# Optimization experiments

Measured on AMD Instinct MI355X. Metric: run time of the kernel, lower is better.

The kernel has to match this reference:

```python
import jax, jax.numpy as jnp
import numpy as np

N_NODES = 100000
N_EDGES = 1200000
IN_CH = 64
HID = 64


def sage_conv(x, src, dst, Wl, b, Wr, num_nodes):
    # mean aggregation of source-node features at target nodes (flow=source_to_target)
    msg = x[src]                                      # [E, C] gather
    agg = jax.ops.segment_sum(msg, dst, num_segments=num_nodes)  # [N, C]
    cnt = jax.ops.segment_sum(jnp.ones((src.shape[0],), x.dtype), dst,
                              num_segments=num_nodes)
    mean = agg / jnp.maximum(cnt, 1.0)[:, None]
    # PyG SAGEConv: lin_l(aggregated) + bias + lin_r(root)
    return mean @ Wl + b + x @ Wr


def setup_inputs() -> dict:
    key = jax.random.key(0)
    ks = jax.random.split(key, 10)
    x = jax.random.normal(ks[0], (N_NODES, IN_CH), dtype=jnp.float32)
    edge_index = jax.random.randint(ks[1], (2, N_EDGES), 0, N_NODES, dtype=jnp.int64)
    s1 = 1.0 / np.sqrt(IN_CH)
    s2 = 1.0 / np.sqrt(HID)
    W1l = jax.random.uniform(ks[2], (IN_CH, HID), jnp.float32, -s1, s1)
    b1 = jax.random.uniform(ks[3], (HID,), jnp.float32, -s1, s1)
    W1r = jax.random.uniform(ks[4], (IN_CH, HID), jnp.float32, -s1, s1)
    W2l = jax.random.uniform(ks[5], (HID, HID), jnp.float32, -s2, s2)
    b2 = jax.random.uniform(ks[6], (HID,), jnp.float32, -s2, s2)
    W2r = jax.random.uniform(ks[7], (HID, HID), jnp.float32, -s2, s2)
    Wfc = jax.random.uniform(ks[8], (HID, 1), jnp.float32, -s2, s2)
    bfc = jax.random.uniform(ks[9], (1,), jnp.float32, -s2, s2)
    return {"x": x, "edge_index": edge_index, "W1l": W1l, "b1": b1, "W1r": W1r,
            "W2l": W2l, "b2": b2, "W2r": W2r, "Wfc": Wfc, "bfc": bfc}


def reference(x, edge_index, W1l, b1, W1r, W2l, b2, W2r, Wfc, bfc):
    num_nodes = x.shape[0]
    src, dst = edge_index[0], edge_index[1]
    x = jnp.nan_to_num(x, nan=0.0)
    # layer 1: SAGEConv -> ReLU (dropout is identity in eval)
    h = jax.nn.relu(sage_conv(x, src, dst, W1l, b1, W1r, num_nodes))
    # layer 2
    h = jax.nn.relu(sage_conv(h, src, dst, W2l, b2, W2r, num_nodes))
    pred = (h @ Wfc + bfc)[:, 0]  # (num_nodes,)
    return pred
```

## Files before the change

### kernel.cpp

```cpp
#include <hip/hip_runtime.h>

#define NN_NODES 100000
#define NN_EDGES 1200000
#define CH 64
#define BUCKET_NODES 200
#define NBUCKETS (NN_NODES / BUCKET_NODES)
#define EPB 4096
#define PASSA_THREADS 1024
#define XCDS 8
#define PCAP 768
#define BMAX (XCDS * PCAP)

typedef __attribute__((ext_vector_type(8))) short bf16x8;
typedef __attribute__((ext_vector_type(4))) float f32x4;

__device__ __forceinline__ float nan0(float v) { return v == v ? v : 0.0f; }

__device__ __forceinline__ unsigned short f2bf(float f) {
    unsigned u = __float_as_uint(f);
    return (unsigned short)((u + 0x7fffu + ((u >> 16) & 1u)) >> 16);
}

__device__ __forceinline__ unsigned xcc_id() {
    unsigned x;
    asm volatile("s_getreg_b32 %0, hwreg(HW_REG_XCC_ID)" : "=s"(x));
    return x & (XCDS - 1);
}

__global__ __launch_bounds__(256) void convert_kernel(
    const float* __restrict__ x, unsigned short* __restrict__ xb, int n4)
{
    int i = blockIdx.x * 256 + threadIdx.x;
    if (i >= n4) return;
    float4 v = ((const float4*)x)[i];
    v.x = nan0(v.x); v.y = nan0(v.y); v.z = nan0(v.z); v.w = nan0(v.w);
    ushort4 o;
    o.x = f2bf(v.x); o.y = f2bf(v.y); o.z = f2bf(v.z); o.w = f2bf(v.w);
    ((ushort4*)xb)[i] = o;
}

__global__ __launch_bounds__(256) void wprep_kernel(
    const float* __restrict__ W1l, const float* __restrict__ W1r,
    const float* __restrict__ W2l, const float* __restrict__ W2r,
    unsigned short* __restrict__ Wt1, unsigned short* __restrict__ Wt2)
{
    int i = blockIdx.x * 256 + threadIdx.x;
    if (i >= 64 * 128) return;
    int n = i >> 7;
    int k = i & 127;
    float v1 = (k < 64) ? W1l[k * 64 + n] : W1r[(k - 64) * 64 + n];
    float v2 = (k < 64) ? W2l[k * 64 + n] : W2r[(k - 64) * 64 + n];
    Wt1[i] = f2bf(v1);
    Wt2[i] = f2bf(v2);
}

__global__ __launch_bounds__(PASSA_THREADS) void passA_kernel(
    const int* __restrict__ src, const int* __restrict__ dst,
    int* __restrict__ bcnt, unsigned int* __restrict__ bbuf, int nEdges)
{
    __shared__ int lhist[NBUCKETS];
    __shared__ int lbase[NBUCKETS];
    int tid = threadIdx.x;
    int e0 = blockIdx.x * EPB;
    unsigned xcc = xcc_id();

    for (int i = tid; i < NBUCKETS; i += PASSA_THREADS) lhist[i] = 0;
    __syncthreads();

    int dreg[4];
    #pragma unroll
    for (int r = 0; r < 4; r++) {
        int e = e0 + r * PASSA_THREADS + tid;
        if (e < nEdges) {
            int d = dst[e];
            dreg[r] = d;
            atomicAdd(&lhist[d / BUCKET_NODES], 1);
        } else {
            dreg[r] = -1;
        }
    }
    __syncthreads();

    for (int i = tid; i < NBUCKETS; i += PASSA_THREADS) {
        int c = lhist[i];
        lbase[i] = c > 0 ? atomicAdd(&bcnt[i * XCDS + xcc], c) : 0;
        lhist[i] = 0;
    }
    __syncthreads();

    #pragma unroll
    for (int r = 0; r < 4; r++) {
        int d = dreg[r];
        if (d >= 0) {
            int e = e0 + r * PASSA_THREADS + tid;
            int s = src[e];
            int b = d / BUCKET_NODES;
            int dloc = d - b * BUCKET_NODES;
            int pos = lbase[b] + atomicAdd(&lhist[b], 1);
            if (pos < PCAP)
                bbuf[((size_t)b * XCDS + xcc) * PCAP + pos] =
                    ((unsigned)dloc << 24) | (unsigned)s;
        }
    }
}

__global__ __launch_bounds__(512) void scan_bcnt_kernel(
    const int* __restrict__ bcnt, int* __restrict__ bbase,
    int* __restrict__ rowptr)
{
    __shared__ int s[512];
    int t = threadIdx.x;
    int own = 0;
    if (t < NBUCKETS) {
        #pragma unroll
        for (int x = 0; x < XCDS; x++) {
            int c = bcnt[t * XCDS + x];
            own += c < PCAP ? c : PCAP;
        }
    }
    s[t] = own;
    __syncthreads();
    for (int off = 1; off < 512; off <<= 1) {
        int v = (t >= off) ? s[t - off] : 0;
        __syncthreads();
        s[t] += v;
        __syncthreads();
    }
    if (t < NBUCKETS) bbase[t] = s[t] - own;
    if (t == NBUCKETS - 1) rowptr[NN_NODES] = s[t];
}

__global__ __launch_bounds__(256) void passB_kernel(
    const int* __restrict__ bcnt, const int* __restrict__ bbase,
    const unsigned int* __restrict__ bbuf,
    int* __restrict__ col, int* __restrict__ rowptr)
{
    __shared__ int hist[BUCKET_NODES];
    __shared__ int cur[BUCKET_NODES];
    __shared__ int sc[256];
    __shared__ unsigned int stage[BMAX];
    int b = blockIdx.x;
    int t = threadIdx.x;
    int base = bbase[b];

    for (int i = t; i < BUCKET_NODES; i += 256) hist[i] = 0;
    __syncthreads();

    int cnt = 0;
    #pragma unroll
    for (int x = 0; x < XCDS; x++) {
        int pc = bcnt[b * XCDS + x];
        if (pc > PCAP) pc = PCAP;
        const unsigned int* seg = bbuf + ((size_t)b * XCDS + x) * PCAP;
        for (int k = t; k < pc; k += 256) {
            unsigned v = seg[k];
            stage[cnt + k] = v;
            atomicAdd(&hist[v >> 24], 1);
        }
        cnt += pc;
    }
    __syncthreads();

    int own = (t < BUCKET_NODES) ? hist[t] : 0;
    sc[t] = own;
    __syncthreads();
    for (int off = 1; off < 256; off <<= 1) {
        int v = (t >= off) ? sc[t - off] : 0;
        __syncthreads();
        sc[t] += v;
        __syncthreads();
    }
    if (t < BUCKET_NODES) {
        int excl = sc[t] - own;
        rowptr[b * BUCKET_NODES + t] = base + excl;
        cur[t] = excl;
    }
    __syncthreads();

    for (int k = t; k < cnt; k += 256) {
        unsigned v = stage[k];
        int dloc = (int)(v >> 24);
        int pos = atomicAdd(&cur[dloc], 1);
        col[base + pos] = (int)(v & 0xFFFFFFu);
    }
}

__global__ __launch_bounds__(256) void gather_kernel(
    const unsigned short* __restrict__ xb,
    const int* __restrict__ rowptr, const int* __restrict__ col,
    unsigned short* __restrict__ mgb, int nNodes)
{
    int w    = threadIdx.x >> 6;
    int lane = threadIdx.x & 63;
    int sub  = lane >> 4;
    int l16  = lane & 15;
    int node = blockIdx.x * 4 + w;
    if (node >= nNodes) return;
    int r0 = rowptr[node], r1 = rowptr[node + 1];
    float a0[4] = {0, 0, 0, 0}, a1[4] = {0, 0, 0, 0};
    int i = r0 + sub;
    for (; i + 4 < r1; i += 8) {
        int s0 = col[i];
        int s1 = col[i + 4];
        uint2 u0 = *(const uint2*)(xb + (size_t)s0 * CH + l16 * 4);
        uint2 u1 = *(const uint2*)(xb + (size_t)s1 * CH + l16 * 4);
        a0[0] += __uint_as_float(u0.x << 16);
        a0[1] += __uint_as_float(u0.x & 0xffff0000u);
        a0[2] += __uint_as_float(u0.y << 16);
        a0[3] += __uint_as_float(u0.y & 0xffff0000u);
        a1[0] += __uint_as_float(u1.x << 16);
        a1[1] += __uint_as_float(u1.x & 0xffff0000u);
        a1[2] += __uint_as_float(u1.y << 16);
        a1[3] += __uint_as_float(u1.y & 0xffff0000u);
    }
    if (i < r1) {
        int s0 = col[i];
        uint2 u0 = *(const uint2*)(xb + (size_t)s0 * CH + l16 * 4);
        a0[0] += __uint_as_float(u0.x << 16);
        a0[1] += __uint_as_float(u0.x & 0xffff0000u);
        a0[2] += __uint_as_float(u0.y << 16);
        a0[3] += __uint_as_float(u0.y & 0xffff0000u);
    }
    #pragma unroll
    for (int j = 0; j < 4; j++) a0[j] += a1[j];
    #pragma unroll
    for (int j = 0; j < 4; j++) {
        a0[j] += __shfl_xor(a0[j], 16, 64);
        a0[j] += __shfl_xor(a0[j], 32, 64);
    }
    if (lane < 16) {
        int deg = r1 - r0;
        float inv = 1.0f / (float)(deg > 0 ? deg : 1);
        ushort4 o;
        o.x = f2bf(a0[0] * inv); o.y = f2bf(a0[1] * inv);
        o.z = f2bf(a0[2] * inv); o.w = f2bf(a0[3] * inv);
        *(ushort4*)(mgb + (size_t)node * CH + l16 * 4) = o;
    }
}

template<int LAYER>
__global__ __launch_bounds__(256) void dense_kernel(
    const unsigned short* __restrict__ rootb,
    const unsigned short* __restrict__ mgb,
    const unsigned short* __restrict__ Wt,
    const float* __restrict__ bias,
    const float* __restrict__ Wfc, const float* __restrict__ bfc,
    unsigned short* __restrict__ hb_out,
    float* __restrict__ out,
    int nNodes)
{
    __shared__ unsigned short sA[64][136];
    __shared__ unsigned short sW[64][136];
    __shared__ unsigned short sO[64][72];

    int tid = threadIdx.x;
    int n_base = blockIdx.x * 64;

    {
        const uint4* g = (const uint4*)Wt;
        for (int i = tid; i < 1024; i += 256) {
            int n = i >> 4;
            int c = i & 15;
            *(uint4*)&sW[n][c * 8] = g[i];
        }
    }
    {
        for (int i = tid; i < 1024; i += 256) {
            int node = i >> 4;
            int c = i & 15;
            int gn = n_base + node;
            if (gn >= nNodes) gn = nNodes - 1;
            const unsigned short* srcp = (c < 8)
                ? (mgb + (size_t)gn * CH + c * 8)
                : (rootb + (size_t)gn * CH + (c - 8) * 8);
            *(uint4*)&sA[node][c * 8] = *(const uint4*)srcp;
        }
    }
    __syncthreads();

    int wave = tid >> 6;
    int lane = tid & 63;
    int quad = lane >> 4;
    int colx = lane & 15;
    int m0 = wave * 16;

    f32x4 acc[4];
    #pragma unroll
    for (int nt = 0; nt < 4; nt++) acc[nt] = (f32x4){0.f, 0.f, 0.f, 0.f};

    #pragma unroll
    for (int ks = 0; ks < 4; ks++) {
        bf16x8 af = *(const bf16x8*)&sA[m0 + colx][ks * 32 + quad * 8];
        #pragma unroll
        for (int nt = 0; nt < 4; nt++) {
            bf16x8 bfr = *(const bf16x8*)&sW[nt * 16 + colx][ks * 32 + quad * 8];
            acc[nt] = __builtin_amdgcn_mfma_f32_16x16x32_bf16(af, bfr, acc[nt], 0, 0, 0);
        }
    }

    float bv[4];
    #pragma unroll
    for (int nt = 0; nt < 4; nt++) bv[nt] = bias[nt * 16 + colx];

    if (LAYER == 1) {
        #pragma unroll
        for (int nt = 0; nt < 4; nt++)
            #pragma unroll
            for (int r = 0; r < 4; r++) {
                float v = acc[nt][r] + bv[nt];
                v = v > 0.f ? v : 0.f;
                sO[m0 + quad * 4 + r][nt * 16 + colx] = f2bf(v);
            }
        __syncthreads();
        for (int i = tid; i < 512; i += 256) {
            int node = i >> 3;
            int c = i & 7;
            int gn = n_base + node;
            if (gn < nNodes)
                *(uint4*)(hb_out + (size_t)gn * CH + c * 8) =
                    *(const uint4*)&sO[node][c * 8];
        }
    } else {
        float wf[4];
        #pragma unroll
        for (int nt = 0; nt < 4; nt++) wf[nt] = Wfc[nt * 16 + colx];
        float bfc0 = bfc[0];
        #pragma unroll
        for (int r = 0; r < 4; r++) {
            float p = 0.f;
            #pragma unroll
            for (int nt = 0; nt < 4; nt++) {
                float v = acc[nt][r] + bv[nt];
                v = v > 0.f ? v : 0.f;
                p += v * wf[nt];
            }
            p += __shfl_xor(p, 1, 64);
            p += __shfl_xor(p, 2, 64);
            p += __shfl_xor(p, 4, 64);
            p += __shfl_xor(p, 8, 64);
            if (colx == 0) {
                int gn = n_base + m0 + quad * 4 + r;
                if (gn < nNodes) out[gn] = p + bfc0;
            }
        }
    }
}

extern "C" void kernel_launch(void* const* d_in, const int* in_sizes, int n_in,
                              void* d_out, int out_size, void* d_ws, size_t ws_size,
                              hipStream_t stream) {
    const float* x    = (const float*)d_in[0];
    const int*   ei   = (const int*)d_in[1];
    const float* W1l  = (const float*)d_in[2];
    const float* b1   = (const float*)d_in[3];
    const float* W1r  = (const float*)d_in[4];
    const float* W2l  = (const float*)d_in[5];
    const float* b2   = (const float*)d_in[6];
    const float* W2r  = (const float*)d_in[7];
    const float* Wfc  = (const float*)d_in[8];
    const float* bfc  = (const float*)d_in[9];
    float* out = (float*)d_out;

    const int N = NN_NODES;
    const int E = NN_EDGES;
    const int* src = ei;
    const int* dst = ei + E;

    char* ws = (char*)d_ws;
    unsigned short* xb  = (unsigned short*)ws;  ws += (size_t)N * CH * sizeof(unsigned short);
    unsigned short* h1b = (unsigned short*)ws;  ws += (size_t)N * CH * sizeof(unsigned short);
    unsigned short* mgb = (unsigned short*)ws;  ws += (size_t)N * CH * sizeof(unsigned short);
    unsigned short* Wt1 = (unsigned short*)ws;  ws += 64 * 128 * sizeof(unsigned short);
    unsigned short* Wt2 = (unsigned short*)ws;  ws += 64 * 128 * sizeof(unsigned short);
    int* bcnt   = (int*)ws;                     ws += (size_t)NBUCKETS * XCDS * sizeof(int);
    int* bbase  = (int*)ws;                     ws += 512 * sizeof(int);
    int* rowptr = (int*)ws;                     ws += (size_t)(N + 1) * sizeof(int);
    int* col    = (int*)ws;                     ws += (size_t)E * sizeof(int);
    unsigned int* bbuf = (unsigned int*)mgb;

    hipMemsetAsync(bcnt, 0, (size_t)NBUCKETS * XCDS * sizeof(int), stream);

    convert_kernel<<<(N * CH / 4 + 255) / 256, 256, 0, stream>>>(x, xb, N * CH / 4);
    wprep_kernel<<<32, 256, 0, stream>>>(W1l, W1r, W2l, W2r, Wt1, Wt2);
    passA_kernel<<<(E + EPB - 1) / EPB, PASSA_THREADS, 0, stream>>>(
        src, dst, bcnt, bbuf, E);
    scan_bcnt_kernel<<<1, 512, 0, stream>>>(bcnt, bbase, rowptr);
    passB_kernel<<<NBUCKETS, 256, 0, stream>>>(bcnt, bbase, bbuf, col, rowptr);

    int gblocks = (N + 3) / 4;
    int dblocks = (N + 63) / 64;

    gather_kernel<<<gblocks, 256, 0, stream>>>(xb, rowptr, col, mgb, N);
    dense_kernel<1><<<dblocks, 256, 0, stream>>>(
        xb, mgb, Wt1, b1, nullptr, nullptr, h1b, nullptr, N);
    gather_kernel<<<gblocks, 256, 0, stream>>>(h1b, rowptr, col, mgb, N);
    dense_kernel<2><<<dblocks, 256, 0, stream>>>(
        h1b, mgb, Wt2, b2, Wfc, bfc, nullptr, out, N);
}
```

Before: 227.6 us.

## Fuse neighbor mean-gather into dense MFMA kernel and vectorize edge bucketing loads

The separate gather kernel and dense kernel are merged, so each 64-node block gathers neighbor means straight into shared memory and then runs the MFMA projection. This removes the write and reread of the intermediate mean buffer and two kernel launches. The cost is that each wave now walks 16 nodes one after another, with fewer blocks in flight to hide gather latency. Separately, passA now loads dst and src as int4, four contiguous edges per thread, and bbuf gets its own workspace region instead of aliasing the mean buffer.

```diff
diff --git a/kernel.cpp b/kernel.cpp
--- a/kernel.cpp
+++ b/kernel.cpp
@@ -67,18 +67,19 @@
     for (int i = tid; i < NBUCKETS; i += PASSA_THREADS) lhist[i] = 0;
     __syncthreads();
 
-    int dreg[4];
-    #pragma unroll
-    for (int r = 0; r < 4; r++) {
-        int e = e0 + r * PASSA_THREADS + tid;
-        if (e < nEdges) {
-            int d = dst[e];
-            dreg[r] = d;
-            atomicAdd(&lhist[d / BUCKET_NODES], 1);
-        } else {
-            dreg[r] = -1;
-        }
-    }
+    int eb = e0 + tid * 4;
+    int nv = nEdges - eb;
+    if (nv > 4) nv = 4;
+    int da[4] = {-1, -1, -1, -1};
+    if (nv == 4) {
+        int4 dv = *(const int4*)(dst + eb);
+        da[0] = dv.x; da[1] = dv.y; da[2] = dv.z; da[3] = dv.w;
+    } else {
+        for (int r = 0; r < nv; r++) da[r] = dst[eb + r];
+    }
+    #pragma unroll
+    for (int r = 0; r < 4; r++)
+        if (da[r] >= 0) atomicAdd(&lhist[da[r] / BUCKET_NODES], 1);
     __syncthreads();
 
     for (int i = tid; i < NBUCKETS; i += PASSA_THREADS) {
@@ -88,18 +89,23 @@
     }
     __syncthreads();
 
+    int sa[4] = {0, 0, 0, 0};
+    if (nv == 4) {
+        int4 sv = *(const int4*)(src + eb);
+        sa[0] = sv.x; sa[1] = sv.y; sa[2] = sv.z; sa[3] = sv.w;
+    } else {
+        for (int r = 0; r < nv; r++) sa[r] = src[eb + r];
+    }
     #pragma unroll
     for (int r = 0; r < 4; r++) {
-        int d = dreg[r];
+        int d = da[r];
         if (d >= 0) {
-            int e = e0 + r * PASSA_THREADS + tid;
-            int s = src[e];
             int b = d / BUCKET_NODES;
             int dloc = d - b * BUCKET_NODES;
             int pos = lbase[b] + atomicAdd(&lhist[b], 1);
             if (pos < PCAP)
                 bbuf[((size_t)b * XCDS + xcc) * PCAP + pos] =
-                    ((unsigned)dloc << 24) | (unsigned)s;
+                    ((unsigned)dloc << 24) | (unsigned)sa[r];
         }
     }
 }
@@ -185,63 +191,10 @@
     }
 }
 
-__global__ __launch_bounds__(256) void gather_kernel(
-    const unsigned short* __restrict__ xb,
+template<int LAYER>
+__global__ __launch_bounds__(256) void fused_kernel(
+    const unsigned short* __restrict__ rootb,
     const int* __restrict__ rowptr, const int* __restrict__ col,
-    unsigned short* __restrict__ mgb, int nNodes)
-{
-    int w    = threadIdx.x >> 6;
-    int lane = threadIdx.x & 63;
-    int sub  = lane >> 4;
-    int l16  = lane & 15;
-    int node = blockIdx.x * 4 + w;
-    if (node >= nNodes) return;
-    int r0 = rowptr[node], r1 = rowptr[node + 1];
-    float a0[4] = {0, 0, 0, 0}, a1[4] = {0, 0, 0, 0};
-    int i = r0 + sub;
-    for (; i + 4 < r1; i += 8) {
-        int s0 = col[i];
-        int s1 = col[i + 4];
-        uint2 u0 = *(const uint2*)(xb + (size_t)s0 * CH + l16 * 4);
-        uint2 u1 = *(const uint2*)(xb + (size_t)s1 * CH + l16 * 4);
-        a0[0] += __uint_as_float(u0.x << 16);
-        a0[1] += __uint_as_float(u0.x & 0xffff0000u);
-        a0[2] += __uint_as_float(u0.y << 16);
-        a0[3] += __uint_as_float(u0.y & 0xffff0000u);
-        a1[0] += __uint_as_float(u1.x << 16);
-        a1[1] += __uint_as_float(u1.x & 0xffff0000u);
-        a1[2] += __uint_as_float(u1.y << 16);
-        a1[3] += __uint_as_float(u1.y & 0xffff0000u);
-    }
-    if (i < r1) {
-        int s0 = col[i];
-        uint2 u0 = *(const uint2*)(xb + (size_t)s0 * CH + l16 * 4);
-        a0[0] += __uint_as_float(u0.x << 16);
-        a0[1] += __uint_as_float(u0.x & 0xffff0000u);
-        a0[2] += __uint_as_float(u0.y << 16);
-        a0[3] += __uint_as_float(u0.y & 0xffff0000u);
-    }
-    #pragma unroll
-    for (int j = 0; j < 4; j++) a0[j] += a1[j];
-    #pragma unroll
-    for (int j = 0; j < 4; j++) {
-        a0[j] += __shfl_xor(a0[j], 16, 64);
-        a0[j] += __shfl_xor(a0[j], 32, 64);
-    }
-    if (lane < 16) {
-        int deg = r1 - r0;
-        float inv = 1.0f / (float)(deg > 0 ? deg : 1);
-        ushort4 o;
-        o.x = f2bf(a0[0] * inv); o.y = f2bf(a0[1] * inv);
-        o.z = f2bf(a0[2] * inv); o.w = f2bf(a0[3] * inv);
-        *(ushort4*)(mgb + (size_t)node * CH + l16 * 4) = o;
-    }
-}
-
-template<int LAYER>
-__global__ __launch_bounds__(256) void dense_kernel(
-    const unsigned short* __restrict__ rootb,
-    const unsigned short* __restrict__ mgb,
     const unsigned short* __restrict__ Wt,
     const float* __restrict__ bias,
     const float* __restrict__ Wfc, const float* __restrict__ bfc,
@@ -264,22 +217,67 @@
             *(uint4*)&sW[n][c * 8] = g[i];
         }
     }
-    {
-        for (int i = tid; i < 1024; i += 256) {
-            int node = i >> 4;
-            int c = i & 15;
-            int gn = n_base + node;
-            if (gn >= nNodes) gn = nNodes - 1;
-            const unsigned short* srcp = (c < 8)
-                ? (mgb + (size_t)gn * CH + c * 8)
-                : (rootb + (size_t)gn * CH + (c - 8) * 8);
-            *(uint4*)&sA[node][c * 8] = *(const uint4*)srcp;
-        }
-    }
-    __syncthreads();
+    for (int i = tid; i < 512; i += 256) {
+        int node = i >> 3;
+        int c = i & 7;
+        int gn = n_base + node;
+        if (gn >= nNodes) gn = nNodes - 1;
+        *(uint4*)&sA[node][64 + c * 8] =
+            *(const uint4*)(rootb + (size_t)gn * CH + c * 8);
+    }
 
     int wave = tid >> 6;
     int lane = tid & 63;
+    int sub  = lane >> 4;
+    int l16  = lane & 15;
+
+    for (int nn = 0; nn < 16; nn++) {
+        int node = wave * 16 + nn;
+        int gn = n_base + node;
+        if (gn >= nNodes) gn = nNodes - 1;
+        int r0 = rowptr[gn], r1 = rowptr[gn + 1];
+        float a0[4] = {0, 0, 0, 0}, a1[4] = {0, 0, 0, 0};
+        int i = r0 + sub;
+        for (; i + 4 < r1; i += 8) {
+            int s0 = col[i];
+            int s1 = col[i + 4];
+            uint2 u0 = *(const uint2*)(rootb + (size_t)s0 * CH + l16 * 4);
+            uint2 u1 = *(const uint2*)(rootb + (size_t)s1 * CH + l16 * 4);
+            a0[0] += __uint_as_float(u0.x << 16);
+            a0[1] += __uint_as_float(u0.x & 0xffff0000u);
+            a0[2] += __uint_as_float(u0.y << 16);
+            a0[3] += __uint_as_float(u0.y & 0xffff0000u);
+            a1[0] += __uint_as_float(u1.x << 16);
+            a1[1] += __uint_as_float(u1.x & 0xffff0000u);
+            a1[2] += __uint_as_float(u1.y << 16);
+            a1[3] += __uint_as_float(u1.y & 0xffff0000u);
+        }
+        if (i < r1) {
+            int s0 = col[i];
+            uint2 u0 = *(const uint2*)(rootb + (size_t)s0 * CH + l16 * 4);
+            a0[0] += __uint_as_float(u0.x << 16);
+            a0[1] += __uint_as_float(u0.x & 0xffff0000u);
+            a0[2] += __uint_as_float(u0.y << 16);
+            a0[3] += __uint_as_float(u0.y & 0xffff0000u);
+        }
+        #pragma unroll
+        for (int j = 0; j < 4; j++) a0[j] += a1[j];
+        #pragma unroll
+        for (int j = 0; j < 4; j++) {
+            a0[j] += __shfl_xor(a0[j], 16, 64);
+            a0[j] += __shfl_xor(a0[j], 32, 64);
+        }
+        if (lane < 16) {
+            int deg = r1 - r0;
+            float inv = 1.0f / (float)(deg > 0 ? deg : 1);
+            ushort4 o;
+            o.x = f2bf(a0[0] * inv); o.y = f2bf(a0[1] * inv);
+            o.z = f2bf(a0[2] * inv); o.w = f2bf(a0[3] * inv);
+            *(ushort4*)&sA[node][l16 * 4] = o;
+        }
+    }
+    __syncthreads();
+
     int quad = lane >> 4;
     int colx = lane & 15;
     int m0 = wave * 16;
@@ -369,14 +367,13 @@
     char* ws = (char*)d_ws;
     unsigned short* xb  = (unsigned short*)ws;  ws += (size_t)N * CH * sizeof(unsigned short);
     unsigned short* h1b = (unsigned short*)ws;  ws += (size_t)N * CH * sizeof(unsigned short);
-    unsigned short* mgb = (unsigned short*)ws;  ws += (size_t)N * CH * sizeof(unsigned short);
     unsigned short* Wt1 = (unsigned short*)ws;  ws += 64 * 128 * sizeof(unsigned short);
     unsigned short* Wt2 = (unsigned short*)ws;  ws += 64 * 128 * sizeof(unsigned short);
     int* bcnt   = (int*)ws;                     ws += (size_t)NBUCKETS * XCDS * sizeof(int);
     int* bbase  = (int*)ws;                     ws += 512 * sizeof(int);
     int* rowptr = (int*)ws;                     ws += (size_t)(N + 1) * sizeof(int);
     int* col    = (int*)ws;                     ws += (size_t)E * sizeof(int);
-    unsigned int* bbuf = (unsigned int*)mgb;
+    unsigned int* bbuf = (unsigned int*)ws;     ws += (size_t)NBUCKETS * XCDS * PCAP * sizeof(unsigned int);
 
     hipMemsetAsync(bcnt, 0, (size_t)NBUCKETS * XCDS * sizeof(int), stream);
 
@@ -387,13 +384,10 @@
     scan_bcnt_kernel<<<1, 512, 0, stream>>>(bcnt, bbase, rowptr);
     passB_kernel<<<NBUCKETS, 256, 0, stream>>>(bcnt, bbase, bbuf, col, rowptr);
 
-    int gblocks = (N + 3) / 4;
     int dblocks = (N + 63) / 64;
 
-    gather_kernel<<<gblocks, 256, 0, stream>>>(xb, rowptr, col, mgb, N);
-    dense_kernel<1><<<dblocks, 256, 0, stream>>>(
-        xb, mgb, Wt1, b1, nullptr, nullptr, h1b, nullptr, N);
-    gather_kernel<<<gblocks, 256, 0, stream>>>(h1b, rowptr, col, mgb, N);
-    dense_kernel<2><<<dblocks, 256, 0, stream>>>(
-        h1b, mgb, Wt2, b2, Wfc, bfc, nullptr, out, N);
-}
+    fused_kernel<1><<<dblocks, 256, 0, stream>>>(
+        xb, rowptr, col, Wt1, b1, nullptr, nullptr, h1b, nullptr, N);
+    fused_kernel<2><<<dblocks, 256, 0, stream>>>(
+        h1b, rowptr, col, Wt2, b2, Wfc, bfc, nullptr, out, N);
+}
```

Measured after the change: 299.4 us. +31.5%, slower.
